# Kernel optimization log

Hardware: AMD Instinct MI355X
Metric: run time of the kernel (lower is better)

Reference implementation:

```python
import jax, jax.numpy as jnp
import numpy as np

B, F, T, H, K = 512, 64, 64, 512, 4  # batch, in_feat, timesteps, hidden, num cells (air0,bed0,air1,bed1)


def setup_inputs() -> dict:
    key = jax.random.key(0)
    ks = jax.random.split(key, 10)
    s = 1.0 / np.sqrt(H)
    u = lambda k, shape: jax.random.uniform(k, shape, jnp.float32, -s, s)
    return {
        "data": jax.random.normal(ks[0], (B, F, T), jnp.float32),
        "init": jax.random.normal(ks[1], (B, H), jnp.float32),
        # stacked params for the 4 branches in order [air0, bed0, air1, bed1]
        "fc_in_W": u(ks[2], (K, H, F)),
        "fc_in_b": u(ks[3], (K, H)),
        "Wih": u(ks[4], (K, 3 * H, H)),   # torch GRUCell weight_ih, gate order r,z,n
        "Whh": u(ks[5], (K, 3 * H, H)),
        "bih": u(ks[6], (K, 3 * H)),
        "bhh": u(ks[7], (K, 3 * H)),
        "fc_out_W": u(ks[8], (2, H)),     # [air, bed] output heads (Linear(512,1))
        "fc_out_b": u(ks[9], (2,)),
    }


def reference(data, init, fc_in_W, fc_in_b, Wih, Whh, bih, bhh, fc_out_W, fc_out_b):
    # Input projections (Linear + ReLU; Dropout is identity in eval): [T, K, B, H]
    proj = jax.nn.relu(jnp.einsum('bft,kof->tkbo', data, fc_in_W) + fc_in_b[None, :, None, :])
    # branches 2,3 (air1, bed1) consume the sequence reversed (data[:, :, 63-i])
    x_seq = jnp.concatenate([proj[:, :2], proj[::-1, 2:]], axis=1)  # [T, K, B, H]

    h0 = jnp.broadcast_to(init[None], (K,) + init.shape)  # all 4 cells start from init

    def step(h, x):  # h, x: [K, B, H]
        gi = jnp.einsum('kbi,koi->kbo', x, Wih) + bih[:, None, :]
        gh = jnp.einsum('kbi,koi->kbo', h, Whh) + bhh[:, None, :]
        ir, iz, inn = jnp.split(gi, 3, axis=-1)
        hr, hz, hn = jnp.split(gh, 3, axis=-1)
        r = jax.nn.sigmoid(ir + hr)
        z = jax.nn.sigmoid(iz + hz)
        n = jnp.tanh(inn + r * hn)
        h_new = (1.0 - z) * n + z * h
        return h_new, h_new

    _, hs = jax.lax.scan(step, h0, x_seq)  # [T, K, B, H]

    # output i (1..64) combines fwd hidden[i] with bwd hidden[65-i] -> reverse bwd stack
    air = hs[:, 0] + hs[::-1, 2]  # [T, B, H]
    bed = hs[:, 1] + hs[::-1, 3]
    air_out = (jnp.einsum('tbh,h->tb', air, fc_out_W[0]) + fc_out_b[0]).T  # [B, T]
    bed_out = (jnp.einsum('tbh,h->tb', bed, fc_out_W[1]) + fc_out_b[1]).T
    return air_out, bed_out
```

## Files before the change

kernel.cpp:

```cpp
#include <hip/hip_runtime.h>
#include <hip/hip_bf16.h>

typedef __hip_bfloat16 bf16;
typedef __attribute__((ext_vector_type(8))) short short8;
typedef __attribute__((ext_vector_type(4))) float f32x4;

#define Hdim 512
#define Bdim 512
#define Tdim 64
#define Fdim 64
#define NC   4

__device__ __forceinline__ float sigmoidf_(float x){ return 1.f/(1.f + __expf(-x)); }
__device__ __forceinline__ float tanhf_(float x){
  float t = __expf(-2.f*fabsf(x));
  float r = (1.f - t)/(1.f + t);
  return copysignf(r, x);
}
__device__ __forceinline__ float bf2f_(short u){
  return __uint_as_float(((unsigned)(unsigned short)u) << 16);
}
__device__ __forceinline__ short f2bf_(float f){
  bf16 b = (bf16)f;
  return *(short*)&b;
}

__global__ __launch_bounds__(256) void pack_kernel(const float* __restrict__ src,
                                                   bf16* __restrict__ dst, int n){
  int idx = (blockIdx.x*256 + threadIdx.x)*4;
  if (idx < n){
    float4 v = *(const float4*)(src + idx);
    dst[idx+0] = (bf16)v.x;
    dst[idx+1] = (bf16)v.y;
    dst[idx+2] = (bf16)v.z;
    dst[idx+3] = (bf16)v.w;
  }
}

__global__ __launch_bounds__(256) void transpose_kernel(const float* __restrict__ data,
                                                        bf16* __restrict__ dataT){
  __shared__ bf16 tile[64*65];
  int b = blockIdx.x;
  int tid = threadIdx.x;
  for (int i = 0; i < 16; ++i){
    int idx = tid + i*256;
    int f = idx >> 6, t = idx & 63;
    tile[f*65 + t] = (bf16)data[(b*64 + f)*64 + t];
  }
  __syncthreads();
  for (int i = 0; i < 16; ++i){
    int idx = tid + i*256;
    int t = idx >> 6, f = idx & 63;
    dataT[(t*Bdim + b)*64 + f] = tile[f*65 + t];
  }
}

__global__ __launch_bounds__(256) void init_kernel(const float* __restrict__ init_h,
                            bf16* __restrict__ h_b1, unsigned* __restrict__ flags){
  int idx = blockIdx.x*256 + threadIdx.x;
  int k = idx >> 18;
  int rem = idx & 262143;
  int bg = rem >> 9;
  int o  = rem & 511;
  int dst = ((k*2 + (bg >> 8))*16 + (o >> 5))*8192 + (bg & 255)*32 + (o & 31);
  h_b1[dst] = (bf16)init_h[rem];
  if (idx < 512) flags[idx] = 0u;
}

__global__ __launch_bounds__(256) void proj_kernel(const bf16* __restrict__ dataT,
    const bf16* __restrict__ fc_in_W, const float* __restrict__ fc_in_b,
    bf16* __restrict__ x_seq){
  __shared__ short ldsA[64*72];
  __shared__ short ldsW[128*72];
  int blk = blockIdx.x;
  int s  = blk >> 7;
  int k  = (blk >> 5) & 3;
  int bt = (blk >> 2) & 7;
  int on = blk & 3;
  int tid = threadIdx.x;
  int lane = tid & 63, wid = tid >> 6;
  int quad = lane >> 4, l16 = lane & 15;
  int src_t = (k < 2) ? s : (Tdim - 1 - s);

  const short* Ag = (const short*)(dataT + (src_t*Bdim + bt*64)*Fdim);
  #pragma unroll
  for (int i = 0; i < 2; ++i){
    int c = tid + i*256; int r = c >> 3, off = c & 7;
    *(int4*)(&ldsA[r*72 + off*8]) = *(const int4*)(&Ag[r*64 + off*8]);
  }
  const short* Wg = (const short*)(fc_in_W + (k*Hdim + on*128)*Fdim);
  #pragma unroll
  for (int i = 0; i < 4; ++i){
    int c = tid + i*256; int r = c >> 3, off = c & 7;
    *(int4*)(&ldsW[r*72 + off*8]) = *(const int4*)(&Wg[r*64 + off*8]);
  }
  __syncthreads();

  f32x4 acc[2][4];
  #pragma unroll
  for (int nt=0; nt<2; ++nt)
    #pragma unroll
    for (int rb=0; rb<4; ++rb) acc[nt][rb] = (f32x4){0.f,0.f,0.f,0.f};

  #pragma unroll
  for (int kk = 0; kk < 2; ++kk){
    int io = kk*32 + quad*8;
    short8 a[4];
    #pragma unroll
    for (int rb=0; rb<4; ++rb) a[rb] = *(const short8*)(&ldsA[(rb*16+l16)*72 + io]);
    #pragma unroll
    for (int nt=0; nt<2; ++nt){
      short8 bw = *(const short8*)(&ldsW[(wid*32 + nt*16 + l16)*72 + io]);
      #pragma unroll
      for (int rb=0; rb<4; ++rb)
        acc[nt][rb] = __builtin_amdgcn_mfma_f32_16x16x32_bf16(a[rb], bw, acc[nt][rb], 0,0,0);
    }
  }

  #pragma unroll
  for (int nt=0; nt<2; ++nt){
    int o = on*128 + wid*32 + nt*16 + l16;
    float bias = fc_in_b[k*Hdim + o];
    #pragma unroll
    for (int rb=0; rb<4; ++rb){
      #pragma unroll
      for (int reg=0; reg<4; ++reg){
        int b = bt*64 + rb*16 + quad*4 + reg;
        float v = acc[nt][rb][reg] + bias;
        v = v > 0.f ? v : 0.f;
        x_seq[((size_t)(s*NC + k)*Bdim + b)*Hdim + o] = (bf16)v;
      }
    }
  }
}

__global__ __launch_bounds__(512) void rnn_kernel(
    const bf16* __restrict__ x_seq, const float* __restrict__ init_h,
    bf16* __restrict__ h_b0, bf16* __restrict__ h_b1,
    const float* __restrict__ Wih, const float* __restrict__ Whh,
    const float* __restrict__ bih, const float* __restrict__ bhh,
    const float* __restrict__ fc_out_W,
    bf16* __restrict__ gi, float* __restrict__ part,
    unsigned* __restrict__ flags, unsigned* __restrict__ xslot)
{
  __shared__ short wlds[3*2*16*512];
  __shared__ int sslot;

  int tid = threadIdx.x;
  int lane = tid & 63, wid = tid >> 6;
  int quad = lane >> 4, l16 = lane & 15;

  unsigned xcc;
  asm volatile("s_getreg_b32 %0, hwreg(HW_REG_XCC_ID)" : "=s"(xcc));
  xcc &= 7u;
  if (tid == 0)
    sslot = (int)__hip_atomic_fetch_add(&xslot[xcc*32], 1u,
                __ATOMIC_RELAXED, __HIP_MEMORY_SCOPE_WORKGROUP);
  __syncthreads();
  int grp = (int)xcc;
  int k   = grp >> 1;
  int bt  = grp & 1;
  int slot = sslot & 31;
  int producer = (slot < 16);
  int j    = slot & 15;
  int obase = j*32;
  int rot  = j;
  unsigned* gflags = flags + grp*32;

  const float* Wsrc = producer ? Wih : Whh;
  for (int i = tid; i < 3*2*16*64; i += 512){
    int plane = i >> 11;
    int rem   = i & 2047;
    int nt    = rem >> 10;
    int rem2  = rem & 1023;
    int kc    = rem2 >> 6;
    int ln    = rem2 & 63;
    int ll16  = ln & 15, lq = ln >> 4;
    const float* srcp = Wsrc +
        ((size_t)(k*3 + plane)*Hdim + obase + nt*16 + ll16)*Hdim + kc*32 + lq*8;
    float4 f0 = *(const float4*)srcp;
    float4 f1 = *(const float4*)(srcp + 4);
    short8 pk;
    pk[0]=f2bf_(f0.x); pk[1]=f2bf_(f0.y); pk[2]=f2bf_(f0.z); pk[3]=f2bf_(f0.w);
    pk[4]=f2bf_(f1.x); pk[5]=f2bf_(f1.y); pk[6]=f2bf_(f1.z); pk[7]=f2bf_(f1.w);
    *(int4*)(&wlds[i*8]) = *(int4*)&pk;
  }

  #define GEMM32X(ABASE) do {                                                   \
    const short* ap0_ = (ABASE) + (wid*32 + l16)*Hdim + quad*8;                 \
    const short* ap1_ = ap0_ + 16*Hdim;                                         \
    short8 ab_[4][2];                                                           \
    _Pragma("unroll")                                                           \
    for (int d=0; d<4; ++d){                                                    \
      int c_ = (d + rot) & 15;                                                  \
      ab_[d][0] = *(const short8*)(ap0_ + c_*32);                               \
      ab_[d][1] = *(const short8*)(ap1_ + c_*32);                               \
    }                                                                           \
    short8 bb_[2][6];                                                           \
    _Pragma("unroll")                                                           \
    for (int p=0; p<6; ++p)                                                     \
      bb_[0][p] = *(const short8*)(&wlds[((p*16 + rot)<<9) + (lane<<3)]);       \
    _Pragma("unroll")                                                           \
    for (int kc=0; kc<16; ++kc){                                                \
      short8 a0_ = ab_[kc&3][0], a1_ = ab_[kc&3][1];                            \
      if (kc < 12){                                                             \
        int c_ = (kc + 4 + rot) & 15;                                           \
        ab_[kc&3][0] = *(const short8*)(ap0_ + c_*32);                          \
        ab_[kc&3][1] = *(const short8*)(ap1_ + c_*32);                          \
      }                                                                         \
      if (kc < 15){                                                             \
        int c_ = (kc + 1 + rot) & 15;                                           \
        _Pragma("unroll")                                                       \
        for (int p=0; p<6; ++p)                                                 \
          bb_[(kc+1)&1][p] = *(const short8*)(&wlds[((p*16 + c_)<<9) + (lane<<3)]); \
      }                                                                         \
      _Pragma("unroll")                                                         \
      for (int g=0; g<3; ++g){                                                  \
        _Pragma("unroll")                                                       \
        for (int nt=0; nt<2; ++nt){                                             \
          short8 bw_ = bb_[kc&1][g*2+nt];                                       \
          acc[g][nt][0] = __builtin_amdgcn_mfma_f32_16x16x32_bf16(a0_, bw_, acc[g][nt][0], 0,0,0); \
          acc[g][nt][1] = __builtin_amdgcn_mfma_f32_16x16x32_bf16(a1_, bw_, acc[g][nt][1], 0,0,0); \
        }                                                                       \
      }                                                                         \
    }                                                                           \
  } while(0)

  #define GEMM32H(HCB) do {                                                     \
    const short* hp0_ = (HCB) + (wid*32 + l16)*32 + quad*8;                     \
    const short* hp1_ = hp0_ + 16*32;                                           \
    short8 ab_[4][2];                                                           \
    _Pragma("unroll")                                                           \
    for (int d=0; d<4; ++d){                                                    \
      int c_ = (d + rot) & 15;                                                  \
      ab_[d][0] = *(const short8*)(hp0_ + c_*8192);                             \
      ab_[d][1] = *(const short8*)(hp1_ + c_*8192);                             \
    }                                                                           \
    short8 bb_[2][6];                                                           \
    _Pragma("unroll")                                                           \
    for (int p=0; p<6; ++p)                                                     \
      bb_[0][p] = *(const short8*)(&wlds[((p*16 + rot)<<9) + (lane<<3)]);       \
    _Pragma("unroll")                                                           \
    for (int kc=0; kc<16; ++kc){                                                \
      short8 a0_ = ab_[kc&3][0], a1_ = ab_[kc&3][1];                            \
      if (kc < 12){                                                             \
        int c_ = (kc + 4 + rot) & 15;                                           \
        ab_[kc&3][0] = *(const short8*)(hp0_ + c_*8192);                        \
        ab_[kc&3][1] = *(const short8*)(hp1_ + c_*8192);                        \
      }                                                                         \
      if (kc < 15){                                                             \
        int c_ = (kc + 1 + rot) & 15;                                           \
        _Pragma("unroll")                                                       \
        for (int p=0; p<6; ++p)                                                 \
          bb_[(kc+1)&1][p] = *(const short8*)(&wlds[((p*16 + c_)<<9) + (lane<<3)]); \
      }                                                                         \
      _Pragma("unroll")                                                         \
      for (int g=0; g<3; ++g){                                                  \
        _Pragma("unroll")                                                       \
        for (int nt=0; nt<2; ++nt){                                             \
          short8 bw_ = bb_[kc&1][g*2+nt];                                       \
          acc[g][nt][0] = __builtin_amdgcn_mfma_f32_16x16x32_bf16(a0_, bw_, acc[g][nt][0], 0,0,0); \
          acc[g][nt][1] = __builtin_amdgcn_mfma_f32_16x16x32_bf16(a1_, bw_, acc[g][nt][1], 0,0,0); \
        }                                                                       \
      }                                                                         \
    }                                                                           \
  } while(0)

  if (producer){
    __syncthreads();
    for (int s = 0; s < 64; ++s){
      f32x4 acc[3][2][2];
      #pragma unroll
      for (int g=0; g<3; ++g)
        #pragma unroll
        for (int nt=0; nt<2; ++nt){
          acc[g][nt][0] = (f32x4){0.f,0.f,0.f,0.f};
          acc[g][nt][1] = (f32x4){0.f,0.f,0.f,0.f};
        }
      if (s >= 3){
        if (wid == 0){
          int g_ = 0;
          while (__hip_atomic_load(&gflags[16 + j], __ATOMIC_RELAXED,
                                   __HIP_MEMORY_SCOPE_AGENT) < (unsigned)(s - 2)){
            __builtin_amdgcn_s_sleep(1);
            if (++g_ > 4000000) break;
          }
        }
        __syncthreads();
      }
      const short* x_base = (const short*)(x_seq + ((size_t)(s*NC + k)*Bdim + bt*256)*Hdim);
      GEMM32X(x_base);
      bf16* gb = gi + ((size_t)(((s % 3)*8 + grp)*16 + j))*24576;
      #pragma unroll
      for (int g=0; g<3; ++g){
        #pragma unroll
        for (int nt=0; nt<2; ++nt){
          short8 pk;
          #pragma unroll
          for (int rb=0; rb<2; ++rb)
            #pragma unroll
            for (int reg=0; reg<4; ++reg)
              pk[rb*4+reg] = f2bf_(acc[g][nt][rb][reg]);
          *(int4*)(gb + ((g*2+nt)*512 + wid*64 + lane)*8) = *(int4*)&pk;
        }
      }
      __syncthreads();
      if (tid == 0)
        __hip_atomic_fetch_add(&gflags[j], 1u,
                               __ATOMIC_RELAXED, __HIP_MEMORY_SCOPE_AGENT);
    }
  } else {
    int o0 = obase + l16, o1 = o0 + 16;
    float br0  = bih[k*3*Hdim + o0] + bhh[k*3*Hdim + o0];
    float br1  = bih[k*3*Hdim + o1] + bhh[k*3*Hdim + o1];
    float bz0  = bih[k*3*Hdim + Hdim + o0] + bhh[k*3*Hdim + Hdim + o0];
    float bz1  = bih[k*3*Hdim + Hdim + o1] + bhh[k*3*Hdim + Hdim + o1];
    float bnx0 = bih[k*3*Hdim + 2*Hdim + o0];
    float bnx1 = bih[k*3*Hdim + 2*Hdim + o1];
    float bnh0 = bhh[k*3*Hdim + 2*Hdim + o0];
    float bnh1 = bhh[k*3*Hdim + 2*Hdim + o1];
    float wout0 = fc_out_W[(k & 1)*Hdim + o0];
    float wout1 = fc_out_W[(k & 1)*Hdim + o1];

    float hk[2][2][4];
    #pragma unroll
    for (int nt=0; nt<2; ++nt)
      #pragma unroll
      for (int rb=0; rb<2; ++rb)
        #pragma unroll
        for (int reg=0; reg<4; ++reg)
          hk[nt][rb][reg] =
            init_h[(bt*256 + wid*32 + rb*16 + quad*4 + reg)*Hdim + obase + nt*16 + l16];

    __syncthreads();

    const int hgrp = (k*2 + bt)*16;

    for (int s = 0; s < 64; ++s){
      const bf16* h_in  = (s & 1) ? h_b0 : h_b1;
      bf16*       h_out = (s & 1) ? h_b1 : h_b0;

      f32x4 acc[3][2][2];
      #pragma unroll
      for (int g=0; g<3; ++g)
        #pragma unroll
        for (int nt=0; nt<2; ++nt){
          acc[g][nt][0] = (f32x4){0.f,0.f,0.f,0.f};
          acc[g][nt][1] = (f32x4){0.f,0.f,0.f,0.f};
        }

      {
        if (wid == 0){
          int g_ = 0;
          for (;;){
            unsigned v_ = 0xFFFFFFFFu, thr_ = 0u;
            if (lane < 16){
              v_ = __hip_atomic_load(&gflags[16 + lane], __ATOMIC_RELAXED,
                                     __HIP_MEMORY_SCOPE_AGENT);
              thr_ = (unsigned)s;
            } else if (lane == 16){
              v_ = __hip_atomic_load(&gflags[j], __ATOMIC_RELAXED,
                                     __HIP_MEMORY_SCOPE_AGENT);
              thr_ = (unsigned)(s + 1);
            }
            if (__ballot(v_ >= thr_) == ~0ull) break;
            __builtin_amdgcn_s_sleep(1);
            if (++g_ > 4000000) break;
          }
        }
        __syncthreads();
      }

      const bf16* gb = gi + ((size_t)(((s % 3)*8 + grp)*16 + j))*24576;
      short8 gv[6];
      #pragma unroll
      for (int p=0; p<6; ++p){
        int4 t = *(const int4*)(gb + (p*512 + wid*64 + lane)*8);
        gv[p] = *(short8*)&t;
      }

      const short* h_cb = (const short*)h_in + (size_t)hgrp*8192;
      GEMM32H(h_cb);

      float hnv[2][2][4];
      bf16* hob = h_out + (size_t)(hgrp + j)*8192;
      #pragma unroll
      for (int rb = 0; rb < 2; ++rb){
        #pragma unroll
        for (int reg = 0; reg < 4; ++reg){
          int bl = wid*32 + rb*16 + quad*4 + reg;
          #pragma unroll
          for (int nt = 0; nt < 2; ++nt){
            float gir = bf2f_(gv[0*2+nt][rb*4+reg]);
            float giz = bf2f_(gv[1*2+nt][rb*4+reg]);
            float gin = bf2f_(gv[2*2+nt][rb*4+reg]);
            float br  = nt ? br1 : br0,  bz = nt ? bz1 : bz0;
            float bnx = nt ? bnx1 : bnx0, bnh = nt ? bnh1 : bnh0;
            float r = sigmoidf_(gir + acc[0][nt][rb][reg] + br);
            float z = sigmoidf_(giz + acc[1][nt][rb][reg] + bz);
            float n = tanhf_(gin + bnx + r*(acc[2][nt][rb][reg] + bnh));
            float hn = (1.f - z)*n + z*hk[nt][rb][reg];
            hk[nt][rb][reg] = hn;
            hnv[nt][rb][reg] = hn;
            hob[bl*32 + nt*16 + l16] = (bf16)hn;
          }
        }
      }

      __syncthreads();
      if (tid == 0)
        __hip_atomic_fetch_add(&gflags[16 + j], 1u,
                               __ATOMIC_RELAXED, __HIP_MEMORY_SCOPE_AGENT);

      int tmap = (k < 2) ? s : (Tdim - 1 - s);
      #pragma unroll
      for (int rb = 0; rb < 2; ++rb){
        #pragma unroll
        for (int reg = 0; reg < 4; ++reg){
          int bl = wid*32 + rb*16 + quad*4 + reg;
          float v = hnv[0][rb][reg]*wout0 + hnv[1][rb][reg]*wout1;
          v += __shfl_xor(v, 1, 64);
          v += __shfl_xor(v, 2, 64);
          v += __shfl_xor(v, 4, 64);
          v += __shfl_xor(v, 8, 64);
          if (l16 == 0)
            __builtin_nontemporal_store(v,
              &part[((size_t)(k*Tdim + tmap)*16 + j)*Bdim + bt*256 + bl]);
        }
      }
    }
  }
  #undef GEMM32X
  #undef GEMM32H
}

__global__ __launch_bounds__(256) void finalize_kernel(const float* __restrict__ part,
                                const float* __restrict__ fc_out_b, float* __restrict__ out){
  int idx = blockIdx.x*256 + threadIdx.x;
  int head = idx >> 15;
  int b = (idx >> 6) & 511;
  int t = idx & 63;
  float v = fc_out_b[head];
  #pragma unroll
  for (int kk = 0; kk < 2; ++kk){
    const float* p = part + (size_t)((head + kk*2)*Tdim + t)*16*Bdim + b;
    #pragma unroll
    for (int jj = 0; jj < 16; ++jj)
      v += p[jj*Bdim];
  }
  out[idx] = v;
}

extern "C" void kernel_launch(void* const* d_in, const int* in_sizes, int n_in,
                              void* d_out, int out_size, void* d_ws, size_t ws_size,
                              hipStream_t stream){
  (void)in_sizes; (void)n_in; (void)out_size; (void)ws_size;
  const float* data     = (const float*)d_in[0];
  const float* init_h   = (const float*)d_in[1];
  const float* fc_in_W  = (const float*)d_in[2];
  const float* fc_in_b  = (const float*)d_in[3];
  const float* Wih      = (const float*)d_in[4];
  const float* Whh      = (const float*)d_in[5];
  const float* bih      = (const float*)d_in[6];
  const float* bhh      = (const float*)d_in[7];
  const float* fc_out_W = (const float*)d_in[8];
  const float* fc_out_b = (const float*)d_in[9];
  float* out = (float*)d_out;

  char* ws = (char*)d_ws;
  bf16*  x_seq   = (bf16*)ws;
  bf16*  h_b0    = (bf16*)(ws + 134217728);
  bf16*  h_b1    = (bf16*)(ws + 136314880);
  bf16*  gi      = (bf16*)(ws + 138412032);
  bf16*  dataT   = (bf16*)(ws + 138412032);
  float* part    = (float*)(ws + 157286400);
  bf16*  fcW_bf  = (bf16*)(ws + 165675008);
  unsigned* flags= (unsigned*)(ws + 165937152);
  unsigned* xslot= (unsigned*)(ws + 165938176);

  const int nFW = NC*Hdim*Fdim;
  hipLaunchKernelGGL(pack_kernel, dim3(nFW/1024), dim3(256), 0, stream, fc_in_W, fcW_bf, nFW);
  hipLaunchKernelGGL(init_kernel, dim3(4096), dim3(256), 0, stream, init_h, h_b1, flags);
  hipLaunchKernelGGL(transpose_kernel, dim3(512), dim3(256), 0, stream, data, dataT);
  hipLaunchKernelGGL(proj_kernel, dim3(8192), dim3(256), 0, stream, dataT, fcW_bf, fc_in_b, x_seq);
  hipLaunchKernelGGL(rnn_kernel, dim3(256), dim3(512), 0, stream,
      x_seq, init_h, h_b0, h_b1, Wih, Whh, bih, bhh, fc_out_W, gi, part, flags, xslot);
  hipLaunchKernelGGL(finalize_kernel, dim3(256), dim3(256), 0, stream, part, fc_out_b, out);
}
```

Measured before the change: 740.7 us.

## Split RNN work into 512 narrower workgroups and fuse output head via atomics

The persistent RNN kernel moves from 256 workgroups of 512 threads, each owning 32 hidden columns, to 512 workgroups of 256 threads, each owning 16 columns, so two workgroups can share a CU. Producer and consumer roles are interleaved by slot parity, and the h buffer layout changes to 16-column chunks. The separate finalize kernel and partial buffer are removed: consumers atomically add their head contributions into the output, which init_kernel pre-fills with the bias. This cuts per-step latency and a launch, but adds more flag polling per step and atomic contention on the output.

New measurement: 1.538 ms. 2.08x slower.

```diff
diff --git a/kernel.cpp b/kernel.cpp
--- a/kernel.cpp
+++ b/kernel.cpp
@@ -56,15 +56,17 @@
 }
 
 __global__ __launch_bounds__(256) void init_kernel(const float* __restrict__ init_h,
-                            bf16* __restrict__ h_b1, unsigned* __restrict__ flags){
+                            bf16* __restrict__ h_b1, unsigned* __restrict__ flags,
+                            float* __restrict__ out, const float* __restrict__ fc_out_b){
   int idx = blockIdx.x*256 + threadIdx.x;
   int k = idx >> 18;
   int rem = idx & 262143;
   int bg = rem >> 9;
   int o  = rem & 511;
-  int dst = ((k*2 + (bg >> 8))*16 + (o >> 5))*8192 + (bg & 255)*32 + (o & 31);
+  int dst = ((k*2 + (bg >> 8))*32 + (o >> 4))*4096 + (bg & 255)*16 + (o & 15);
   h_b1[dst] = (bf16)init_h[rem];
-  if (idx < 512) flags[idx] = 0u;
+  if (idx < 2048) flags[idx] = 0u;
+  if (idx < 65536) out[idx] = fc_out_b[idx >> 15];
 }
 
 __global__ __launch_bounds__(256) void proj_kernel(const bf16* __restrict__ dataT,
@@ -134,50 +136,47 @@
   }
 }
 
-__global__ __launch_bounds__(512) void rnn_kernel(
+__global__ __launch_bounds__(256, 2) void rnn_kernel(
     const bf16* __restrict__ x_seq, const float* __restrict__ init_h,
     bf16* __restrict__ h_b0, bf16* __restrict__ h_b1,
     const float* __restrict__ Wih, const float* __restrict__ Whh,
     const float* __restrict__ bih, const float* __restrict__ bhh,
     const float* __restrict__ fc_out_W,
-    bf16* __restrict__ gi, float* __restrict__ part,
+    float* __restrict__ out, bf16* __restrict__ gi,
     unsigned* __restrict__ flags, unsigned* __restrict__ xslot)
 {
-  __shared__ short wlds[3*2*16*512];
+  __shared__ short wlds[3*16*512 + 4096];
   __shared__ int sslot;
 
   int tid = threadIdx.x;
-  int lane = tid & 63, wid = tid >> 6;
+  int lane = tid & 63, w = tid >> 6;
   int quad = lane >> 4, l16 = lane & 15;
 
   unsigned xcc;
   asm volatile("s_getreg_b32 %0, hwreg(HW_REG_XCC_ID)" : "=s"(xcc));
   xcc &= 7u;
   if (tid == 0)
-    sslot = (int)__hip_atomic_fetch_add(&xslot[xcc*32], 1u,
-                __ATOMIC_RELAXED, __HIP_MEMORY_SCOPE_WORKGROUP);
+    sslot = (int)__hip_atomic_fetch_add(&xslot[xcc*16], 1u,
+                __ATOMIC_RELAXED, __HIP_MEMORY_SCOPE_AGENT);
   __syncthreads();
   int grp = (int)xcc;
   int k   = grp >> 1;
   int bt  = grp & 1;
-  int slot = sslot & 31;
-  int producer = (slot < 16);
-  int j    = slot & 15;
-  int obase = j*32;
-  int rot  = j;
-  unsigned* gflags = flags + grp*32;
+  int slot = sslot & 63;
+  int producer = !(slot & 1);
+  int j    = slot >> 1;
+  int rot  = j & 15;
+  unsigned* gflags = flags + grp*64;
 
   const float* Wsrc = producer ? Wih : Whh;
-  for (int i = tid; i < 3*2*16*64; i += 512){
-    int plane = i >> 11;
-    int rem   = i & 2047;
-    int nt    = rem >> 10;
-    int rem2  = rem & 1023;
-    int kc    = rem2 >> 6;
-    int ln    = rem2 & 63;
-    int ll16  = ln & 15, lq = ln >> 4;
+  for (int i = tid; i < 3072; i += 256){
+    int g   = i >> 10;
+    int rem = i & 1023;
+    int kc  = rem >> 6;
+    int ln  = rem & 63;
+    int ll16 = ln & 15, lq = ln >> 4;
     const float* srcp = Wsrc +
-        ((size_t)(k*3 + plane)*Hdim + obase + nt*16 + ll16)*Hdim + kc*32 + lq*8;
+        ((size_t)(k*3 + g)*Hdim + j*16 + ll16)*Hdim + kc*32 + lq*8;
     float4 f0 = *(const float4*)srcp;
     float4 f1 = *(const float4*)(srcp + 4);
     short8 pk;
@@ -185,124 +184,79 @@
     pk[4]=f2bf_(f1.x); pk[5]=f2bf_(f1.y); pk[6]=f2bf_(f1.z); pk[7]=f2bf_(f1.w);
     *(int4*)(&wlds[i*8]) = *(int4*)&pk;
   }
-
-  #define GEMM32X(ABASE) do {                                                   \
-    const short* ap0_ = (ABASE) + (wid*32 + l16)*Hdim + quad*8;                 \
-    const short* ap1_ = ap0_ + 16*Hdim;                                         \
-    short8 ab_[4][2];                                                           \
+  __syncthreads();
+
+  const size_t hgbase = (size_t)grp * 131072;
+
+  #define GEMM16(AP0, ASTRIDEF, ACHUNK, ACC) do {                               \
     _Pragma("unroll")                                                           \
-    for (int d=0; d<4; ++d){                                                    \
-      int c_ = (d + rot) & 15;                                                  \
-      ab_[d][0] = *(const short8*)(ap0_ + c_*32);                               \
-      ab_[d][1] = *(const short8*)(ap1_ + c_*32);                               \
-    }                                                                           \
-    short8 bb_[2][6];                                                           \
+    for (int g=0; g<3; ++g)                                                     \
+      _Pragma("unroll")                                                         \
+      for (int f=0; f<4; ++f) ACC[g][f] = (f32x4){0.f,0.f,0.f,0.f};             \
+    short8 ab_[2][4];                                                           \
+    short8 bb_[2][3];                                                           \
     _Pragma("unroll")                                                           \
-    for (int p=0; p<6; ++p)                                                     \
-      bb_[0][p] = *(const short8*)(&wlds[((p*16 + rot)<<9) + (lane<<3)]);       \
+    for (int f=0; f<4; ++f)                                                     \
+      ab_[0][f] = *(const short8*)((AP0) + f*(ASTRIDEF) + (size_t)rot*(ACHUNK));\
+    _Pragma("unroll")                                                           \
+    for (int g=0; g<3; ++g)                                                     \
+      bb_[0][g] = *(const short8*)(&wlds[((g*16 + rot)<<9) + (lane<<3)]);       \
     _Pragma("unroll")                                                           \
     for (int kc=0; kc<16; ++kc){                                                \
-      short8 a0_ = ab_[kc&3][0], a1_ = ab_[kc&3][1];                            \
-      if (kc < 12){                                                             \
-        int c_ = (kc + 4 + rot) & 15;                                           \
-        ab_[kc&3][0] = *(const short8*)(ap0_ + c_*32);                          \
-        ab_[kc&3][1] = *(const short8*)(ap1_ + c_*32);                          \
-      }                                                                         \
       if (kc < 15){                                                             \
         int c_ = (kc + 1 + rot) & 15;                                           \
         _Pragma("unroll")                                                       \
-        for (int p=0; p<6; ++p)                                                 \
-          bb_[(kc+1)&1][p] = *(const short8*)(&wlds[((p*16 + c_)<<9) + (lane<<3)]); \
+        for (int f=0; f<4; ++f)                                                 \
+          ab_[(kc+1)&1][f] = *(const short8*)((AP0) + f*(ASTRIDEF) + (size_t)c_*(ACHUNK)); \
+        _Pragma("unroll")                                                       \
+        for (int g=0; g<3; ++g)                                                 \
+          bb_[(kc+1)&1][g] = *(const short8*)(&wlds[((g*16 + c_)<<9) + (lane<<3)]); \
       }                                                                         \
       _Pragma("unroll")                                                         \
       for (int g=0; g<3; ++g){                                                  \
+        short8 bw_ = bb_[kc&1][g];                                              \
         _Pragma("unroll")                                                       \
-        for (int nt=0; nt<2; ++nt){                                             \
-          short8 bw_ = bb_[kc&1][g*2+nt];                                       \
-          acc[g][nt][0] = __builtin_amdgcn_mfma_f32_16x16x32_bf16(a0_, bw_, acc[g][nt][0], 0,0,0); \
-          acc[g][nt][1] = __builtin_amdgcn_mfma_f32_16x16x32_bf16(a1_, bw_, acc[g][nt][1], 0,0,0); \
-        }                                                                       \
+        for (int f=0; f<4; ++f)                                                 \
+          ACC[g][f] = __builtin_amdgcn_mfma_f32_16x16x32_bf16(ab_[kc&1][f], bw_, ACC[g][f], 0,0,0); \
       }                                                                         \
     }                                                                           \
   } while(0)
 
-  #define GEMM32H(HCB) do {                                                     \
-    const short* hp0_ = (HCB) + (wid*32 + l16)*32 + quad*8;                     \
-    const short* hp1_ = hp0_ + 16*32;                                           \
-    short8 ab_[4][2];                                                           \
-    _Pragma("unroll")                                                           \
-    for (int d=0; d<4; ++d){                                                    \
-      int c_ = (d + rot) & 15;                                                  \
-      ab_[d][0] = *(const short8*)(hp0_ + c_*8192);                             \
-      ab_[d][1] = *(const short8*)(hp1_ + c_*8192);                             \
-    }                                                                           \
-    short8 bb_[2][6];                                                           \
-    _Pragma("unroll")                                                           \
-    for (int p=0; p<6; ++p)                                                     \
-      bb_[0][p] = *(const short8*)(&wlds[((p*16 + rot)<<9) + (lane<<3)]);       \
-    _Pragma("unroll")                                                           \
-    for (int kc=0; kc<16; ++kc){                                                \
-      short8 a0_ = ab_[kc&3][0], a1_ = ab_[kc&3][1];                            \
-      if (kc < 12){                                                             \
-        int c_ = (kc + 4 + rot) & 15;                                           \
-        ab_[kc&3][0] = *(const short8*)(hp0_ + c_*8192);                        \
-        ab_[kc&3][1] = *(const short8*)(hp1_ + c_*8192);                        \
-      }                                                                         \
-      if (kc < 15){                                                             \
-        int c_ = (kc + 1 + rot) & 15;                                           \
-        _Pragma("unroll")                                                       \
-        for (int p=0; p<6; ++p)                                                 \
-          bb_[(kc+1)&1][p] = *(const short8*)(&wlds[((p*16 + c_)<<9) + (lane<<3)]); \
-      }                                                                         \
-      _Pragma("unroll")                                                         \
-      for (int g=0; g<3; ++g){                                                  \
-        _Pragma("unroll")                                                       \
-        for (int nt=0; nt<2; ++nt){                                             \
-          short8 bw_ = bb_[kc&1][g*2+nt];                                       \
-          acc[g][nt][0] = __builtin_amdgcn_mfma_f32_16x16x32_bf16(a0_, bw_, acc[g][nt][0], 0,0,0); \
-          acc[g][nt][1] = __builtin_amdgcn_mfma_f32_16x16x32_bf16(a1_, bw_, acc[g][nt][1], 0,0,0); \
-        }                                                                       \
-      }                                                                         \
-    }                                                                           \
-  } while(0)
+  #define PKU(a,b) ( ((unsigned)(unsigned short)f2bf_(a)) | (((unsigned)(unsigned short)f2bf_(b))<<16) )
 
   if (producer){
-    __syncthreads();
-    for (int s = 0; s < 64; ++s){
-      f32x4 acc[3][2][2];
-      #pragma unroll
-      for (int g=0; g<3; ++g)
-        #pragma unroll
-        for (int nt=0; nt<2; ++nt){
-          acc[g][nt][0] = (f32x4){0.f,0.f,0.f,0.f};
-          acc[g][nt][1] = (f32x4){0.f,0.f,0.f,0.f};
-        }
-      if (s >= 3){
-        if (wid == 0){
+    for (int t = 0; t < 64; ++t){
+      if (t >= 3){
+        if (w == 0){
           int g_ = 0;
-          while (__hip_atomic_load(&gflags[16 + j], __ATOMIC_RELAXED,
-                                   __HIP_MEMORY_SCOPE_AGENT) < (unsigned)(s - 2)){
+          while (__hip_atomic_load(&gflags[32 + j], __ATOMIC_RELAXED,
+                                   __HIP_MEMORY_SCOPE_AGENT) < (unsigned)(t - 2)){
             __builtin_amdgcn_s_sleep(1);
-            if (++g_ > 4000000) break;
+            if (++g_ > 8000000) break;
           }
         }
         __syncthreads();
       }
-      const short* x_base = (const short*)(x_seq + ((size_t)(s*NC + k)*Bdim + bt*256)*Hdim);
-      GEMM32X(x_base);
-      bf16* gb = gi + ((size_t)(((s % 3)*8 + grp)*16 + j))*24576;
-      #pragma unroll
-      for (int g=0; g<3; ++g){
-        #pragma unroll
-        for (int nt=0; nt<2; ++nt){
-          short8 pk;
-          #pragma unroll
-          for (int rb=0; rb<2; ++rb)
-            #pragma unroll
-            for (int reg=0; reg<4; ++reg)
-              pk[rb*4+reg] = f2bf_(acc[g][nt][rb][reg]);
-          *(int4*)(gb + ((g*2+nt)*512 + wid*64 + lane)*8) = *(int4*)&pk;
-        }
+      f32x4 acc[3][4];
+      const short* xb = (const short*)(x_seq +
+          ((size_t)(t*NC + k)*Bdim + bt*256)*Hdim);
+      const short* ap0 = xb + (w*64 + l16)*Hdim + quad*8;
+      GEMM16(ap0, 16*Hdim, 32, acc);
+
+      bf16* gb = gi + ((size_t)(((t % 3)*8 + grp)*32 + j))*12288;
+      #pragma unroll
+      for (int g = 0; g < 3; ++g){
+        int4 q0, q1;
+        q0.x = (int)PKU(acc[g][0][0], acc[g][0][1]);
+        q0.y = (int)PKU(acc[g][0][2], acc[g][0][3]);
+        q0.z = (int)PKU(acc[g][1][0], acc[g][1][1]);
+        q0.w = (int)PKU(acc[g][1][2], acc[g][1][3]);
+        q1.x = (int)PKU(acc[g][2][0], acc[g][2][1]);
+        q1.y = (int)PKU(acc[g][2][2], acc[g][2][3]);
+        q1.z = (int)PKU(acc[g][3][0], acc[g][3][1]);
+        q1.w = (int)PKU(acc[g][3][2], acc[g][3][3]);
+        *(int4*)(gb + (g*256 + tid)*16)     = q0;
+        *(int4*)(gb + (g*256 + tid)*16 + 8) = q1;
       }
       __syncthreads();
       if (tid == 0)
@@ -310,145 +264,104 @@
                                __ATOMIC_RELAXED, __HIP_MEMORY_SCOPE_AGENT);
     }
   } else {
-    int o0 = obase + l16, o1 = o0 + 16;
-    float br0  = bih[k*3*Hdim + o0] + bhh[k*3*Hdim + o0];
-    float br1  = bih[k*3*Hdim + o1] + bhh[k*3*Hdim + o1];
-    float bz0  = bih[k*3*Hdim + Hdim + o0] + bhh[k*3*Hdim + Hdim + o0];
-    float bz1  = bih[k*3*Hdim + Hdim + o1] + bhh[k*3*Hdim + Hdim + o1];
-    float bnx0 = bih[k*3*Hdim + 2*Hdim + o0];
-    float bnx1 = bih[k*3*Hdim + 2*Hdim + o1];
-    float bnh0 = bhh[k*3*Hdim + 2*Hdim + o0];
-    float bnh1 = bhh[k*3*Hdim + 2*Hdim + o1];
-    float wout0 = fc_out_W[(k & 1)*Hdim + o0];
-    float wout1 = fc_out_W[(k & 1)*Hdim + o1];
-
-    float hk[2][2][4];
+    int o0 = j*16 + l16;
+    float br  = bih[k*3*Hdim + o0] + bhh[k*3*Hdim + o0];
+    float bz  = bih[k*3*Hdim + Hdim + o0] + bhh[k*3*Hdim + Hdim + o0];
+    float bnx = bih[k*3*Hdim + 2*Hdim + o0];
+    float bnh = bhh[k*3*Hdim + 2*Hdim + o0];
+    float wout = fc_out_W[(k & 1)*Hdim + o0];
+    int head = k & 1;
+
+    float hk[4][4];
     #pragma unroll
-    for (int nt=0; nt<2; ++nt)
-      #pragma unroll
-      for (int rb=0; rb<2; ++rb)
-        #pragma unroll
-        for (int reg=0; reg<4; ++reg)
-          hk[nt][rb][reg] =
-            init_h[(bt*256 + wid*32 + rb*16 + quad*4 + reg)*Hdim + obase + nt*16 + l16];
-
-    __syncthreads();
-
-    const int hgrp = (k*2 + bt)*16;
+    for (int f=0; f<4; ++f)
+      #pragma unroll
+      for (int reg=0; reg<4; ++reg)
+        hk[f][reg] =
+          init_h[(bt*256 + w*64 + f*16 + quad*4 + reg)*Hdim + o0];
 
     for (int s = 0; s < 64; ++s){
       const bf16* h_in  = (s & 1) ? h_b0 : h_b1;
       bf16*       h_out = (s & 1) ? h_b1 : h_b0;
 
-      f32x4 acc[3][2][2];
-      #pragma unroll
-      for (int g=0; g<3; ++g)
-        #pragma unroll
-        for (int nt=0; nt<2; ++nt){
-          acc[g][nt][0] = (f32x4){0.f,0.f,0.f,0.f};
-          acc[g][nt][1] = (f32x4){0.f,0.f,0.f,0.f};
+      if (w == 0){
+        int g_ = 0;
+        for (;;){
+          unsigned v_ = 0xFFFFFFFFu, thr_ = 0u;
+          if (lane < 32){
+            v_ = __hip_atomic_load(&gflags[32 + lane], __ATOMIC_RELAXED,
+                                   __HIP_MEMORY_SCOPE_AGENT);
+            thr_ = (unsigned)s;
+          } else if (lane == 32){
+            v_ = __hip_atomic_load(&gflags[j], __ATOMIC_RELAXED,
+                                   __HIP_MEMORY_SCOPE_AGENT);
+            thr_ = (unsigned)(s + 1);
+          }
+          if (__ballot(v_ >= thr_) == ~0ull) break;
+          __builtin_amdgcn_s_sleep(1);
+          if (++g_ > 8000000) break;
         }
-
-      {
-        if (wid == 0){
-          int g_ = 0;
-          for (;;){
-            unsigned v_ = 0xFFFFFFFFu, thr_ = 0u;
-            if (lane < 16){
-              v_ = __hip_atomic_load(&gflags[16 + lane], __ATOMIC_RELAXED,
-                                     __HIP_MEMORY_SCOPE_AGENT);
-              thr_ = (unsigned)s;
-            } else if (lane == 16){
-              v_ = __hip_atomic_load(&gflags[j], __ATOMIC_RELAXED,
-                                     __HIP_MEMORY_SCOPE_AGENT);
-              thr_ = (unsigned)(s + 1);
-            }
-            if (__ballot(v_ >= thr_) == ~0ull) break;
-            __builtin_amdgcn_s_sleep(1);
-            if (++g_ > 4000000) break;
-          }
-        }
-        __syncthreads();
-      }
-
-      const bf16* gb = gi + ((size_t)(((s % 3)*8 + grp)*16 + j))*24576;
-      short8 gv[6];
-      #pragma unroll
-      for (int p=0; p<6; ++p){
-        int4 t = *(const int4*)(gb + (p*512 + wid*64 + lane)*8);
-        gv[p] = *(short8*)&t;
-      }
-
-      const short* h_cb = (const short*)h_in + (size_t)hgrp*8192;
-      GEMM32H(h_cb);
-
-      float hnv[2][2][4];
-      bf16* hob = h_out + (size_t)(hgrp + j)*8192;
-      #pragma unroll
-      for (int rb = 0; rb < 2; ++rb){
+      }
+      __syncthreads();
+
+      const bf16* gb = gi + ((size_t)(((s % 3)*8 + grp)*32 + j))*12288;
+      int4 gq[3][2];
+      #pragma unroll
+      for (int g = 0; g < 3; ++g){
+        gq[g][0] = *(const int4*)(gb + (g*256 + tid)*16);
+        gq[g][1] = *(const int4*)(gb + (g*256 + tid)*16 + 8);
+      }
+
+      f32x4 hacc[3][4];
+      const short* hcb = (const short*)h_in + hgbase;
+      const short* hp0 = hcb + (quad>>1)*4096 + (w*64 + l16)*16 + (quad&1)*8;
+      GEMM16(hp0, 256, 8192, hacc);
+
+      bf16* hob = h_out + hgbase + (size_t)j*4096;
+      #pragma unroll
+      for (int f = 0; f < 4; ++f){
         #pragma unroll
         for (int reg = 0; reg < 4; ++reg){
-          int bl = wid*32 + rb*16 + quad*4 + reg;
-          #pragma unroll
-          for (int nt = 0; nt < 2; ++nt){
-            float gir = bf2f_(gv[0*2+nt][rb*4+reg]);
-            float giz = bf2f_(gv[1*2+nt][rb*4+reg]);
-            float gin = bf2f_(gv[2*2+nt][rb*4+reg]);
-            float br  = nt ? br1 : br0,  bz = nt ? bz1 : bz0;
-            float bnx = nt ? bnx1 : bnx0, bnh = nt ? bnh1 : bnh0;
-            float r = sigmoidf_(gir + acc[0][nt][rb][reg] + br);
-            float z = sigmoidf_(giz + acc[1][nt][rb][reg] + bz);
-            float n = tanhf_(gin + bnx + r*(acc[2][nt][rb][reg] + bnh));
-            float hn = (1.f - z)*n + z*hk[nt][rb][reg];
-            hk[nt][rb][reg] = hn;
-            hnv[nt][rb][reg] = hn;
-            hob[bl*32 + nt*16 + l16] = (bf16)hn;
-          }
+          int4 q0 = gq[0][f>>1], q1 = gq[1][f>>1], q2 = gq[2][f>>1];
+          const int wsel = (f & 1)*2 + (reg >> 1);
+          unsigned u0 = (unsigned)((wsel==0)? q0.x : (wsel==1)? q0.y : (wsel==2)? q0.z : q0.w);
+          unsigned u1 = (unsigned)((wsel==0)? q1.x : (wsel==1)? q1.y : (wsel==2)? q1.z : q1.w);
+          unsigned u2 = (unsigned)((wsel==0)? q2.x : (wsel==1)? q2.y : (wsel==2)? q2.z : q2.w);
+          float gir = bf2f_((short)((reg & 1) ? (u0 >> 16) : (u0 & 0xFFFFu)));
+          float giz = bf2f_((short)((reg & 1) ? (u1 >> 16) : (u1 & 0xFFFFu)));
+          float gin = bf2f_((short)((reg & 1) ? (u2 >> 16) : (u2 & 0xFFFFu)));
+          float r = sigmoidf_(gir + hacc[0][f][reg] + br);
+          float z = sigmoidf_(giz + hacc[1][f][reg] + bz);
+          float n = tanhf_(gin + bnx + r*(hacc[2][f][reg] + bnh));
+          float hn = (1.f - z)*n + z*hk[f][reg];
+          hk[f][reg] = hn;
+          hob[(w*64 + f*16 + quad*4 + reg)*16 + l16] = (bf16)hn;
         }
       }
 
       __syncthreads();
       if (tid == 0)
-        __hip_atomic_fetch_add(&gflags[16 + j], 1u,
+        __hip_atomic_fetch_add(&gflags[32 + j], 1u,
                                __ATOMIC_RELAXED, __HIP_MEMORY_SCOPE_AGENT);
 
       int tmap = (k < 2) ? s : (Tdim - 1 - s);
       #pragma unroll
-      for (int rb = 0; rb < 2; ++rb){
+      for (int f = 0; f < 4; ++f){
         #pragma unroll
         for (int reg = 0; reg < 4; ++reg){
-          int bl = wid*32 + rb*16 + quad*4 + reg;
-          float v = hnv[0][rb][reg]*wout0 + hnv[1][rb][reg]*wout1;
+          float v = hk[f][reg]*wout;
           v += __shfl_xor(v, 1, 64);
           v += __shfl_xor(v, 2, 64);
           v += __shfl_xor(v, 4, 64);
           v += __shfl_xor(v, 8, 64);
           if (l16 == 0)
-            __builtin_nontemporal_store(v,
-              &part[((size_t)(k*Tdim + tmap)*16 + j)*Bdim + bt*256 + bl]);
+            atomicAdd(&out[((head << 9) + bt*256 + w*64 + f*16 + quad*4 + reg)*64 + tmap], v);
         }
       }
     }
   }
-  #undef GEMM32X
-  #undef GEMM32H
-}
-
-__global__ __launch_bounds__(256) void finalize_kernel(const float* __restrict__ part,
-                                const float* __restrict__ fc_out_b, float* __restrict__ out){
-  int idx = blockIdx.x*256 + threadIdx.x;
-  int head = idx >> 15;
-  int b = (idx >> 6) & 511;
-  int t = idx & 63;
-  float v = fc_out_b[head];
-  #pragma unroll
-  for (int kk = 0; kk < 2; ++kk){
-    const float* p = part + (size_t)((head + kk*2)*Tdim + t)*16*Bdim + b;
-    #pragma unroll
-    for (int jj = 0; jj < 16; ++jj)
-      v += p[jj*Bdim];
-  }
-  out[idx] = v;
+  #undef GEMM16
+  #undef PKU
 }
 
 extern "C" void kernel_launch(void* const* d_in, const int* in_sizes, int n_in,
@@ -473,17 +386,16 @@
   bf16*  h_b1    = (bf16*)(ws + 136314880);
   bf16*  gi      = (bf16*)(ws + 138412032);
   bf16*  dataT   = (bf16*)(ws + 138412032);
-  float* part    = (float*)(ws + 157286400);
+  unsigned* flags= (unsigned*)(ws + 157286400);
+  unsigned* xslot= (unsigned*)(ws + 157290496);
   bf16*  fcW_bf  = (bf16*)(ws + 165675008);
-  unsigned* flags= (unsigned*)(ws + 165937152);
-  unsigned* xslot= (unsigned*)(ws + 165938176);
 
   const int nFW = NC*Hdim*Fdim;
   hipLaunchKernelGGL(pack_kernel, dim3(nFW/1024), dim3(256), 0, stream, fc_in_W, fcW_bf, nFW);
-  hipLaunchKernelGGL(init_kernel, dim3(4096), dim3(256), 0, stream, init_h, h_b1, flags);
+  hipLaunchKernelGGL(init_kernel, dim3(4096), dim3(256), 0, stream,
+      init_h, h_b1, flags, out, fc_out_b);
   hipLaunchKernelGGL(transpose_kernel, dim3(512), dim3(256), 0, stream, data, dataT);
   hipLaunchKernelGGL(proj_kernel, dim3(8192), dim3(256), 0, stream, dataT, fcW_bf, fc_in_b, x_seq);
-  hipLaunchKernelGGL(rnn_kernel, dim3(256), dim3(512), 0, stream,
-      x_seq, init_h, h_b0, h_b1, Wih, Whh, bih, bhh, fc_out_W, gi, part, flags, xslot);
-  hipLaunchKernelGGL(finalize_kernel, dim3(256), dim3(256), 0, stream, part, fc_out_b, out);
-}
+  hipLaunchKernelGGL(rnn_kernel, dim3(512), dim3(256), 0, stream,
+      x_seq, init_h, h_b0, h_b1, Wih, Whh, bih, bhh, fc_out_W, out, gi, flags, xslot);
+}
```

## Retile RNN GEMM warps to 64x16 tiles and accumulate output heads atomically

Applied to the files above, without the earlier changes.

Each of the 8 warps now covers a 64-row by 16-column output tile (4 M-warps × 2 N-warps) instead of a 32-row by 32-column one. Each warp reads only its own half of the weight planes from LDS, which halves the B-operand LDS traffic but doubles A-operand loads from global memory for x and h. The gate-input buffer layout changes to match the new tiling, and launch bounds now request 2 blocks per SM. The output-head partial sums are written with atomicAdd into a buffer that init_kernel zeroes, replacing plain stores. This adds atomic traffic, and the zeroing covers idx*2 floats, so its coverage of the whole part buffer is uncertain.

Result: slower. 1.214 ms (+63.9%).

```diff
diff --git a/kernel.cpp b/kernel.cpp
--- a/kernel.cpp
+++ b/kernel.cpp
@@ -56,7 +56,8 @@
 }
 
 __global__ __launch_bounds__(256) void init_kernel(const float* __restrict__ init_h,
-                            bf16* __restrict__ h_b1, unsigned* __restrict__ flags){
+                            bf16* __restrict__ h_b1, unsigned* __restrict__ flags,
+                            float* __restrict__ part){
   int idx = blockIdx.x*256 + threadIdx.x;
   int k = idx >> 18;
   int rem = idx & 262143;
@@ -65,6 +66,8 @@
   int dst = ((k*2 + (bg >> 8))*16 + (o >> 5))*8192 + (bg & 255)*32 + (o & 31);
   h_b1[dst] = (bf16)init_h[rem];
   if (idx < 512) flags[idx] = 0u;
+  float2 z; z.x = 0.f; z.y = 0.f;
+  ((float2*)part)[idx] = z;
 }
 
 __global__ __launch_bounds__(256) void proj_kernel(const bf16* __restrict__ dataT,
@@ -134,7 +137,7 @@
   }
 }
 
-__global__ __launch_bounds__(512) void rnn_kernel(
+__global__ __launch_bounds__(512, 2) void rnn_kernel(
     const bf16* __restrict__ x_seq, const float* __restrict__ init_h,
     bf16* __restrict__ h_b0, bf16* __restrict__ h_b1,
     const float* __restrict__ Wih, const float* __restrict__ Whh,
@@ -149,6 +152,8 @@
   int tid = threadIdx.x;
   int lane = tid & 63, wid = tid >> 6;
   int quad = lane >> 4, l16 = lane & 15;
+  int wgm = wid & 3;
+  int wgn = wid >> 2;
 
   unsigned xcc;
   asm volatile("s_getreg_b32 %0, hwreg(HW_REG_XCC_ID)" : "=s"(xcc));
@@ -186,97 +191,56 @@
     *(int4*)(&wlds[i*8]) = *(int4*)&pk;
   }
 
-  #define GEMM32X(ABASE) do {                                                   \
-    const short* ap0_ = (ABASE) + (wid*32 + l16)*Hdim + quad*8;                 \
-    const short* ap1_ = ap0_ + 16*Hdim;                                         \
-    short8 ab_[4][2];                                                           \
+  #define GEMM64(AP, RS, CS) do {                                               \
+    short8 ab_[4][4];                                                           \
     _Pragma("unroll")                                                           \
     for (int d=0; d<4; ++d){                                                    \
       int c_ = (d + rot) & 15;                                                  \
-      ab_[d][0] = *(const short8*)(ap0_ + c_*32);                               \
-      ab_[d][1] = *(const short8*)(ap1_ + c_*32);                               \
+      _Pragma("unroll")                                                         \
+      for (int f=0; f<4; ++f)                                                   \
+        ab_[d][f] = *(const short8*)((AP) + f*16*(RS) + (size_t)c_*(CS));       \
     }                                                                           \
-    short8 bb_[2][6];                                                           \
+    short8 bb_[2][3];                                                           \
     _Pragma("unroll")                                                           \
-    for (int p=0; p<6; ++p)                                                     \
-      bb_[0][p] = *(const short8*)(&wlds[((p*16 + rot)<<9) + (lane<<3)]);       \
+    for (int g=0; g<3; ++g)                                                     \
+      bb_[0][g] = *(const short8*)(&wlds[(((g*2+wgn)*16 + rot)<<9) + (lane<<3)]);\
     _Pragma("unroll")                                                           \
     for (int kc=0; kc<16; ++kc){                                                \
-      short8 a0_ = ab_[kc&3][0], a1_ = ab_[kc&3][1];                            \
+      short8 a_[4];                                                             \
+      _Pragma("unroll")                                                         \
+      for (int f=0; f<4; ++f) a_[f] = ab_[kc&3][f];                             \
       if (kc < 12){                                                             \
         int c_ = (kc + 4 + rot) & 15;                                           \
-        ab_[kc&3][0] = *(const short8*)(ap0_ + c_*32);                          \
-        ab_[kc&3][1] = *(const short8*)(ap1_ + c_*32);                          \
+        _Pragma("unroll")                                                       \
+        for (int f=0; f<4; ++f)                                                 \
+          ab_[kc&3][f] = *(const short8*)((AP) + f*16*(RS) + (size_t)c_*(CS));  \
       }                                                                         \
       if (kc < 15){                                                             \
         int c_ = (kc + 1 + rot) & 15;                                           \
         _Pragma("unroll")                                                       \
-        for (int p=0; p<6; ++p)                                                 \
-          bb_[(kc+1)&1][p] = *(const short8*)(&wlds[((p*16 + c_)<<9) + (lane<<3)]); \
+        for (int g=0; g<3; ++g)                                                 \
+          bb_[(kc+1)&1][g] = *(const short8*)(&wlds[(((g*2+wgn)*16 + c_)<<9) + (lane<<3)]); \
       }                                                                         \
       _Pragma("unroll")                                                         \
       for (int g=0; g<3; ++g){                                                  \
+        short8 bw_ = bb_[kc&1][g];                                              \
         _Pragma("unroll")                                                       \
-        for (int nt=0; nt<2; ++nt){                                             \
-          short8 bw_ = bb_[kc&1][g*2+nt];                                       \
-          acc[g][nt][0] = __builtin_amdgcn_mfma_f32_16x16x32_bf16(a0_, bw_, acc[g][nt][0], 0,0,0); \
-          acc[g][nt][1] = __builtin_amdgcn_mfma_f32_16x16x32_bf16(a1_, bw_, acc[g][nt][1], 0,0,0); \
-        }                                                                       \
+        for (int f=0; f<4; ++f)                                                 \
+          acc[g][f] = __builtin_amdgcn_mfma_f32_16x16x32_bf16(a_[f], bw_, acc[g][f], 0,0,0); \
       }                                                                         \
     }                                                                           \
   } while(0)
 
-  #define GEMM32H(HCB) do {                                                     \
-    const short* hp0_ = (HCB) + (wid*32 + l16)*32 + quad*8;                     \
-    const short* hp1_ = hp0_ + 16*32;                                           \
-    short8 ab_[4][2];                                                           \
-    _Pragma("unroll")                                                           \
-    for (int d=0; d<4; ++d){                                                    \
-      int c_ = (d + rot) & 15;                                                  \
-      ab_[d][0] = *(const short8*)(hp0_ + c_*8192);                             \
-      ab_[d][1] = *(const short8*)(hp1_ + c_*8192);                             \
-    }                                                                           \
-    short8 bb_[2][6];                                                           \
-    _Pragma("unroll")                                                           \
-    for (int p=0; p<6; ++p)                                                     \
-      bb_[0][p] = *(const short8*)(&wlds[((p*16 + rot)<<9) + (lane<<3)]);       \
-    _Pragma("unroll")                                                           \
-    for (int kc=0; kc<16; ++kc){                                                \
-      short8 a0_ = ab_[kc&3][0], a1_ = ab_[kc&3][1];                            \
-      if (kc < 12){                                                             \
-        int c_ = (kc + 4 + rot) & 15;                                           \
-        ab_[kc&3][0] = *(const short8*)(hp0_ + c_*8192);                        \
-        ab_[kc&3][1] = *(const short8*)(hp1_ + c_*8192);                        \
-      }                                                                         \
-      if (kc < 15){                                                             \
-        int c_ = (kc + 1 + rot) & 15;                                           \
-        _Pragma("unroll")                                                       \
-        for (int p=0; p<6; ++p)                                                 \
-          bb_[(kc+1)&1][p] = *(const short8*)(&wlds[((p*16 + c_)<<9) + (lane<<3)]); \
-      }                                                                         \
-      _Pragma("unroll")                                                         \
-      for (int g=0; g<3; ++g){                                                  \
-        _Pragma("unroll")                                                       \
-        for (int nt=0; nt<2; ++nt){                                             \
-          short8 bw_ = bb_[kc&1][g*2+nt];                                       \
-          acc[g][nt][0] = __builtin_amdgcn_mfma_f32_16x16x32_bf16(a0_, bw_, acc[g][nt][0], 0,0,0); \
-          acc[g][nt][1] = __builtin_amdgcn_mfma_f32_16x16x32_bf16(a1_, bw_, acc[g][nt][1], 0,0,0); \
-        }                                                                       \
-      }                                                                         \
-    }                                                                           \
-  } while(0)
+  #define PKU(a,b) ( ((unsigned)(unsigned short)f2bf_(a)) | (((unsigned)(unsigned short)f2bf_(b))<<16) )
 
   if (producer){
     __syncthreads();
     for (int s = 0; s < 64; ++s){
-      f32x4 acc[3][2][2];
+      f32x4 acc[3][4];
       #pragma unroll
       for (int g=0; g<3; ++g)
         #pragma unroll
-        for (int nt=0; nt<2; ++nt){
-          acc[g][nt][0] = (f32x4){0.f,0.f,0.f,0.f};
-          acc[g][nt][1] = (f32x4){0.f,0.f,0.f,0.f};
-        }
+        for (int f=0; f<4; ++f) acc[g][f] = (f32x4){0.f,0.f,0.f,0.f};
       if (s >= 3){
         if (wid == 0){
           int g_ = 0;
@@ -289,19 +253,18 @@
         __syncthreads();
       }
       const short* x_base = (const short*)(x_seq + ((size_t)(s*NC + k)*Bdim + bt*256)*Hdim);
-      GEMM32X(x_base);
+      const short* ap = x_base + (wgm*64 + l16)*Hdim + quad*8;
+      GEMM64(ap, Hdim, 32);
+
       bf16* gb = gi + ((size_t)(((s % 3)*8 + grp)*16 + j))*24576;
       #pragma unroll
       for (int g=0; g<3; ++g){
         #pragma unroll
-        for (int nt=0; nt<2; ++nt){
-          short8 pk;
-          #pragma unroll
-          for (int rb=0; rb<2; ++rb)
-            #pragma unroll
-            for (int reg=0; reg<4; ++reg)
-              pk[rb*4+reg] = f2bf_(acc[g][nt][rb][reg]);
-          *(int4*)(gb + ((g*2+nt)*512 + wid*64 + lane)*8) = *(int4*)&pk;
+        for (int f=0; f<4; ++f){
+          int2 q;
+          q.x = (int)PKU(acc[g][f][0], acc[g][f][1]);
+          q.y = (int)PKU(acc[g][f][2], acc[g][f][3]);
+          *(int2*)(gb + ((g*4 + f)*512 + wid*64 + lane)*4) = q;
         }
       }
       __syncthreads();
@@ -310,27 +273,20 @@
                                __ATOMIC_RELAXED, __HIP_MEMORY_SCOPE_AGENT);
     }
   } else {
-    int o0 = obase + l16, o1 = o0 + 16;
-    float br0  = bih[k*3*Hdim + o0] + bhh[k*3*Hdim + o0];
-    float br1  = bih[k*3*Hdim + o1] + bhh[k*3*Hdim + o1];
-    float bz0  = bih[k*3*Hdim + Hdim + o0] + bhh[k*3*Hdim + Hdim + o0];
-    float bz1  = bih[k*3*Hdim + Hdim + o1] + bhh[k*3*Hdim + Hdim + o1];
-    float bnx0 = bih[k*3*Hdim + 2*Hdim + o0];
-    float bnx1 = bih[k*3*Hdim + 2*Hdim + o1];
-    float bnh0 = bhh[k*3*Hdim + 2*Hdim + o0];
-    float bnh1 = bhh[k*3*Hdim + 2*Hdim + o1];
-    float wout0 = fc_out_W[(k & 1)*Hdim + o0];
-    float wout1 = fc_out_W[(k & 1)*Hdim + o1];
-
-    float hk[2][2][4];
-    #pragma unroll
-    for (int nt=0; nt<2; ++nt)
-      #pragma unroll
-      for (int rb=0; rb<2; ++rb)
-        #pragma unroll
-        for (int reg=0; reg<4; ++reg)
-          hk[nt][rb][reg] =
-            init_h[(bt*256 + wid*32 + rb*16 + quad*4 + reg)*Hdim + obase + nt*16 + l16];
+    int o0 = obase + wgn*16 + l16;
+    float br  = bih[k*3*Hdim + o0] + bhh[k*3*Hdim + o0];
+    float bz  = bih[k*3*Hdim + Hdim + o0] + bhh[k*3*Hdim + Hdim + o0];
+    float bnx = bih[k*3*Hdim + 2*Hdim + o0];
+    float bnh = bhh[k*3*Hdim + 2*Hdim + o0];
+    float wout = fc_out_W[(k & 1)*Hdim + o0];
+
+    float hk[4][4];
+    #pragma unroll
+    for (int f=0; f<4; ++f)
+      #pragma unroll
+      for (int reg=0; reg<4; ++reg)
+        hk[f][reg] =
+          init_h[(bt*256 + wgm*64 + f*16 + quad*4 + reg)*Hdim + o0];
 
     __syncthreads();
 
@@ -340,14 +296,11 @@
       const bf16* h_in  = (s & 1) ? h_b0 : h_b1;
       bf16*       h_out = (s & 1) ? h_b1 : h_b0;
 
-      f32x4 acc[3][2][2];
+      f32x4 acc[3][4];
       #pragma unroll
       for (int g=0; g<3; ++g)
         #pragma unroll
-        for (int nt=0; nt<2; ++nt){
-          acc[g][nt][0] = (f32x4){0.f,0.f,0.f,0.f};
-          acc[g][nt][1] = (f32x4){0.f,0.f,0.f,0.f};
-        }
+        for (int f=0; f<4; ++f) acc[g][f] = (f32x4){0.f,0.f,0.f,0.f};
 
       {
         if (wid == 0){
@@ -372,38 +325,35 @@
       }
 
       const bf16* gb = gi + ((size_t)(((s % 3)*8 + grp)*16 + j))*24576;
-      short8 gv[6];
-      #pragma unroll
-      for (int p=0; p<6; ++p){
-        int4 t = *(const int4*)(gb + (p*512 + wid*64 + lane)*8);
-        gv[p] = *(short8*)&t;
-      }
+      int2 gq[3][4];
+      #pragma unroll
+      for (int g=0; g<3; ++g)
+        #pragma unroll
+        for (int f=0; f<4; ++f)
+          gq[g][f] = *(const int2*)(gb + ((g*4 + f)*512 + wid*64 + lane)*4);
 
       const short* h_cb = (const short*)h_in + (size_t)hgrp*8192;
-      GEMM32H(h_cb);
-
-      float hnv[2][2][4];
+      const short* hp = h_cb + (wgm*64 + l16)*32 + quad*8;
+      GEMM64(hp, 32, 8192);
+
       bf16* hob = h_out + (size_t)(hgrp + j)*8192;
       #pragma unroll
-      for (int rb = 0; rb < 2; ++rb){
+      for (int f = 0; f < 4; ++f){
         #pragma unroll
         for (int reg = 0; reg < 4; ++reg){
-          int bl = wid*32 + rb*16 + quad*4 + reg;
-          #pragma unroll
-          for (int nt = 0; nt < 2; ++nt){
-            float gir = bf2f_(gv[0*2+nt][rb*4+reg]);
-            float giz = bf2f_(gv[1*2+nt][rb*4+reg]);
-            float gin = bf2f_(gv[2*2+nt][rb*4+reg]);
-            float br  = nt ? br1 : br0,  bz = nt ? bz1 : bz0;
-            float bnx = nt ? bnx1 : bnx0, bnh = nt ? bnh1 : bnh0;
-            float r = sigmoidf_(gir + acc[0][nt][rb][reg] + br);
-            float z = sigmoidf_(giz + acc[1][nt][rb][reg] + bz);
-            float n = tanhf_(gin + bnx + r*(acc[2][nt][rb][reg] + bnh));
-            float hn = (1.f - z)*n + z*hk[nt][rb][reg];
-            hk[nt][rb][reg] = hn;
-            hnv[nt][rb][reg] = hn;
-            hob[bl*32 + nt*16 + l16] = (bf16)hn;
-          }
+          int bl = wgm*64 + f*16 + quad*4 + reg;
+          unsigned ur = (unsigned)((reg & 2) ? gq[0][f].y : gq[0][f].x);
+          unsigned uz = (unsigned)((reg & 2) ? gq[1][f].y : gq[1][f].x);
+          unsigned un = (unsigned)((reg & 2) ? gq[2][f].y : gq[2][f].x);
+          float gir = bf2f_((short)((reg & 1) ? (ur >> 16) : (ur & 0xFFFFu)));
+          float giz = bf2f_((short)((reg & 1) ? (uz >> 16) : (uz & 0xFFFFu)));
+          float gin = bf2f_((short)((reg & 1) ? (un >> 16) : (un & 0xFFFFu)));
+          float r = sigmoidf_(gir + acc[0][f][reg] + br);
+          float z = sigmoidf_(giz + acc[1][f][reg] + bz);
+          float n = tanhf_(gin + bnx + r*(acc[2][f][reg] + bnh));
+          float hn = (1.f - z)*n + z*hk[f][reg];
+          hk[f][reg] = hn;
+          hob[bl*32 + wgn*16 + l16] = (bf16)hn;
         }
       }
 
@@ -414,24 +364,23 @@
 
       int tmap = (k < 2) ? s : (Tdim - 1 - s);
       #pragma unroll
-      for (int rb = 0; rb < 2; ++rb){
+      for (int f = 0; f < 4; ++f){
         #pragma unroll
         for (int reg = 0; reg < 4; ++reg){
-          int bl = wid*32 + rb*16 + quad*4 + reg;
-          float v = hnv[0][rb][reg]*wout0 + hnv[1][rb][reg]*wout1;
+          int bl = wgm*64 + f*16 + quad*4 + reg;
+          float v = hk[f][reg]*wout;
           v += __shfl_xor(v, 1, 64);
           v += __shfl_xor(v, 2, 64);
           v += __shfl_xor(v, 4, 64);
           v += __shfl_xor(v, 8, 64);
           if (l16 == 0)
-            __builtin_nontemporal_store(v,
-              &part[((size_t)(k*Tdim + tmap)*16 + j)*Bdim + bt*256 + bl]);
+            atomicAdd(&part[((size_t)(k*Tdim + tmap)*16 + j)*Bdim + bt*256 + bl], v);
         }
       }
     }
   }
-  #undef GEMM32X
-  #undef GEMM32H
+  #undef GEMM64
+  #undef PKU
 }
 
 __global__ __launch_bounds__(256) void finalize_kernel(const float* __restrict__ part,
@@ -480,7 +429,7 @@
 
   const int nFW = NC*Hdim*Fdim;
   hipLaunchKernelGGL(pack_kernel, dim3(nFW/1024), dim3(256), 0, stream, fc_in_W, fcW_bf, nFW);
-  hipLaunchKernelGGL(init_kernel, dim3(4096), dim3(256), 0, stream, init_h, h_b1, flags);
+  hipLaunchKernelGGL(init_kernel, dim3(4096), dim3(256), 0, stream, init_h, h_b1, flags, part);
   hipLaunchKernelGGL(transpose_kernel, dim3(512), dim3(256), 0, stream, data, dataT);
   hipLaunchKernelGGL(proj_kernel, dim3(8192), dim3(256), 0, stream, dataT, fcW_bf, fc_in_b, x_seq);
   hipLaunchKernelGGL(rnn_kernel, dim3(256), dim3(512), 0, stream,
```
